# Kernel tuning notes

Hardware: AMD Instinct MI355X
Metric: run time of the kernel (lower is better)

## Reference

```python
import jax, jax.numpy as jnp
import numpy as np

S, N, IN_F, OUT_F = 8, 2048, 256, 64
SLOPE = 0.1
NEG_INF = -9e15


def leaky_relu(x, slope=SLOPE):
    return jnp.where(x >= 0, x, slope * x)


def setup_inputs() -> dict:
    key = jax.random.key(0)
    k1, k2, k3, k4, k5, k6 = jax.random.split(key, 6)
    inDoc = jax.random.normal(k1, (S, N, IN_F), dtype=jnp.float32)
    adj = jax.random.randint(k2, (S, N, N, 1), 0, 2, dtype=jnp.int32)
    # Linear(inFeat, outFeat): weight [outFeat, inFeat], bias [outFeat]
    W_w = jax.random.normal(k3, (OUT_F, IN_F), dtype=jnp.float32) / np.sqrt(IN_F)
    W_b = jax.random.normal(k4, (OUT_F,), dtype=jnp.float32) * 0.01
    # Linear(2*outFeat, 1): weight [1, 2*outFeat], bias [1]
    a_w = jax.random.normal(k5, (1, 2 * OUT_F), dtype=jnp.float32) / np.sqrt(2 * OUT_F)
    a_b = jax.random.normal(k6, (1,), dtype=jnp.float32) * 0.01
    return {"inDoc": inDoc, "adj": adj, "W_w": W_w, "W_b": W_b, "a_w": a_w, "a_b": a_b}


def reference(inDoc, adj, W_w, W_b, a_w, a_b):
    # h: [S, N, F]
    h = jnp.einsum('snd,fd->snf', inDoc, W_w) + W_b
    F_ = h.shape[-1]
    # aParams(concat(h_i, h_j)) == h_i @ a1 + h_j @ a2 + b  (exact same affine map)
    a1 = a_w[0, :F_]
    a2 = a_w[0, F_:]
    score_i = jnp.einsum('snf,f->sn', h, a1)  # [S, N]
    score_j = jnp.einsum('snf,f->sn', h, a2)  # [S, N]
    att = score_i[:, :, None] + score_j[:, None, :] + a_b[0]  # [S, N, N]
    att = leaky_relu(att)
    m = adj[..., 0]  # [S, N, N]
    att = jnp.where((m == 0) | (m == -1), jnp.float32(NEG_INF), att)
    att = jax.nn.softmax(att, axis=2)  # normalize over neighbors j
    h_out = leaky_relu(jnp.einsum('sij,sjf->sif', att, h))
    return (h_out, att)
```

## Files before the change

kernel.cpp:

```cpp
#include <hip/hip_runtime.h>

#define SLOPE 0.1f
#define NEG_INF_F (-9000000000000000.0f)

typedef int            iv4    __attribute__((ext_vector_type(4)));
typedef float          fv4    __attribute__((ext_vector_type(4)));
typedef unsigned short u16;
typedef u16            u16v4  __attribute__((ext_vector_type(4)));
typedef __bf16         bf16x8 __attribute__((ext_vector_type(8)));

static __device__ __forceinline__ u16 f2bf(float x) {
    union { float f; unsigned u; } v; v.f = x;
    unsigned r = v.u + 0x7fffu + ((v.u >> 16) & 1u);
    return (u16)(r >> 16);
}

static __device__ __forceinline__ void lds_barrier() {
    asm volatile("s_waitcnt lgkmcnt(0)" ::: "memory");
    __builtin_amdgcn_s_barrier();
}


__global__ void k_wt(const float* __restrict__ W, float* __restrict__ wT) {
    int idx = blockIdx.x * 256 + threadIdx.x;
    int k = idx >> 6, f = idx & 63;
    wT[idx] = W[f * 256 + k];
}

__global__ __launch_bounds__(256) void k_h(
    const float* __restrict__ inDoc, const float* __restrict__ wT,
    const float* __restrict__ Wb, const float* __restrict__ aw,
    u16* __restrict__ hT, float* __restrict__ si, float* __restrict__ sj)
{
    __shared__ float wTl[32 * 64];
    __shared__ float inl[32][36];
    const int t  = threadIdx.x;
    const int R0 = blockIdx.x * 32;
    const int fq = t & 15, rq = t >> 4;
    const int f0 = fq << 2;

    float acc[2][4];
#pragma unroll
    for (int r = 0; r < 2; ++r)
#pragma unroll
        for (int c = 0; c < 4; ++c) acc[r][c] = 0.f;

    for (int kc = 0; kc < 8; ++kc) {
        __syncthreads();
        {
            const float4* src = (const float4*)(wT + kc * 2048);
            float4 a = src[t * 2], b = src[t * 2 + 1];
            ((float4*)wTl)[t * 2]     = a;
            ((float4*)wTl)[t * 2 + 1] = b;
        }
        {
            int r = t >> 3, q = t & 7;
            const float* src = inDoc + (size_t)(R0 + r) * 256 + kc * 32 + q * 4;
            *(float4*)&inl[r][q * 4] = *(const float4*)src;
        }
        __syncthreads();
#pragma unroll
        for (int k4 = 0; k4 < 8; ++k4) {
            const int k0 = k4 << 2;
            float w[4][4];
#pragma unroll
            for (int j = 0; j < 4; ++j) {
                float4 wv = *(const float4*)&wTl[(k0 + j) * 64 + f0];
                w[j][0] = wv.x; w[j][1] = wv.y; w[j][2] = wv.z; w[j][3] = wv.w;
            }
#pragma unroll
            for (int r = 0; r < 2; ++r) {
                float4 av = *(const float4*)&inl[rq * 2 + r][k0];
                float a[4] = {av.x, av.y, av.z, av.w};
#pragma unroll
                for (int j = 0; j < 4; ++j)
#pragma unroll
                    for (int c = 0; c < 4; ++c)
                        acc[r][c] = fmaf(a[j], w[j][c], acc[r][c]);
            }
        }
    }

    float bw[4], a1[4], a2[4];
#pragma unroll
    for (int c = 0; c < 4; ++c) {
        bw[c] = Wb[f0 + c];
        a1[c] = aw[f0 + c];
        a2[c] = aw[64 + f0 + c];
    }
    float sip[2], sjp[2];
#pragma unroll
    for (int r = 0; r < 2; ++r) {
#pragma unroll
        for (int c = 0; c < 4; ++c) acc[r][c] += bw[c];
        float x = 0.f, y = 0.f;
#pragma unroll
        for (int c = 0; c < 4; ++c) {
            x = fmaf(acc[r][c], a1[c], x);
            y = fmaf(acc[r][c], a2[c], y);
        }
        sip[r] = x; sjp[r] = y;
    }
#pragma unroll
    for (int m = 1; m <= 8; m <<= 1) {
#pragma unroll
        for (int r = 0; r < 2; ++r) {
            sip[r] += __shfl_xor(sip[r], m, 64);
            sjp[r] += __shfl_xor(sjp[r], m, 64);
        }
    }
    const int rowbase = R0 + rq * 2;
    const int sR = rowbase >> 11;
    const int il = rowbase & 2047;
    u16* hTp = hT + (size_t)sR * 131072;
#pragma unroll
    for (int r = 0; r < 2; ++r)
#pragma unroll
        for (int c = 0; c < 4; ++c)
            hTp[(size_t)(f0 + c) * 2048 + il + r] = f2bf(acc[r][c]);
    if (fq == 0) {
#pragma unroll
        for (int r = 0; r < 2; ++r) {
            si[rowbase + r] = sip[r];
            sj[rowbase + r] = sjp[r];
        }
    }
}

__global__ __launch_bounds__(512, 2) void k_att(
    const int* __restrict__ adj, const u16* __restrict__ hT,
    const float* __restrict__ si, const float* __restrict__ sj,
    const float* __restrict__ ab_p,
    float* __restrict__ out_h, float* __restrict__ out_att)
{
    __shared__ __align__(16) u16 pB[16 * 2048];
    __shared__ __align__(16) float red[4][64][4];
    const int t    = threadIdx.x;
    const int lane = t & 63, wv = t >> 6;
    const int i0   = blockIdx.x * 16;
    const int s    = i0 >> 11;
    const float ab = ab_p[0];
    const float* sjb = sj + (size_t)s * 2048;

    fv4 sv[8];
#pragma unroll
    for (int c = 0; c < 8; ++c)
        sv[c] = *(const fv4*)(sjb + c * 256 + lane * 4);

    const int r0  = wv * 2,      r1  = r0 + 1;
    const int fr0 = i0 + r0,     fr1 = i0 + r1;
    const float si0 = si[fr0] + ab;
    const float si1 = si[fr1] + ab;
    const int* a0 = adj + (size_t)fr0 * 2048;
    const int* a1 = adj + (size_t)fr1 * 2048;

    iv4 m0[8], m1[8];
#pragma unroll
    for (int c = 0; c < 8; ++c)
        m0[c] = __builtin_nontemporal_load((const iv4*)(a0 + c * 256 + lane * 4));
#pragma unroll
    for (int c = 0; c < 8; ++c)
        m1[c] = __builtin_nontemporal_load((const iv4*)(a1 + c * 256 + lane * 4));

#pragma unroll
    for (int rr = 0; rr < 2; ++rr) {
        const int r  = rr ? r1 : r0;
        const int fr = rr ? fr1 : fr0;
        const float sival = rr ? si1 : si0;
        iv4* mm = rr ? m1 : m0;
        float v[32];
#pragma unroll
        for (int c = 0; c < 8; ++c) {
            iv4 m = mm[c];
            float x;
            x = sival + sv[c].x; x = fmaxf(x, SLOPE * x);
            v[c*4+0] = (m.x == 0 || m.x == -1) ? NEG_INF_F : x;
            x = sival + sv[c].y; x = fmaxf(x, SLOPE * x);
            v[c*4+1] = (m.y == 0 || m.y == -1) ? NEG_INF_F : x;
            x = sival + sv[c].z; x = fmaxf(x, SLOPE * x);
            v[c*4+2] = (m.z == 0 || m.z == -1) ? NEG_INF_F : x;
            x = sival + sv[c].w; x = fmaxf(x, SLOPE * x);
            v[c*4+3] = (m.w == 0 || m.w == -1) ? NEG_INF_F : x;
        }
        float mx = v[0];
#pragma unroll
        for (int q = 1; q < 32; ++q) mx = fmaxf(mx, v[q]);
#pragma unroll
        for (int m2 = 1; m2 < 64; m2 <<= 1) mx = fmaxf(mx, __shfl_xor(mx, m2, 64));
        float sum = 0.f;
#pragma unroll
        for (int q = 0; q < 32; ++q) { v[q] = __expf(v[q] - mx); sum += v[q]; }
#pragma unroll
        for (int m2 = 1; m2 < 64; m2 <<= 1) sum += __shfl_xor(sum, m2, 64);
        const float inv = 1.0f / sum;

        float* attrow = out_att + (size_t)fr * 2048;
        const unsigned swz = (unsigned)(r & 7) << 4;
#pragma unroll
        for (int c = 0; c < 8; ++c) {
            const int j = c * 256 + lane * 4;
            fv4 pv;
            pv.x = v[c*4+0] * inv; pv.y = v[c*4+1] * inv;
            pv.z = v[c*4+2] * inv; pv.w = v[c*4+3] * inv;
            *(fv4*)(attrow + j) = pv;
            u16v4 pk;
            pk.x = f2bf(pv.x); pk.y = f2bf(pv.y);
            pk.z = f2bf(pv.z); pk.w = f2bf(pv.w);
            unsigned byte = ((unsigned)(r * 4096 + j * 2)) ^ swz;
            *(u16v4*)((char*)pB + byte) = pk;
        }
    }
    lds_barrier();

    const int fq    = wv & 3;
    const int kh    = wv >> 2;
    const int m16   = lane & 15;
    const int klane = lane >> 4;
    const unsigned sw = (unsigned)(lane & 7) << 4;
    const __bf16* hTs = (const __bf16*)hT + (size_t)s * 131072
                      + (size_t)(fq * 16 + m16) * 2048 + kh * 1024 + klane * 8;
    const unsigned bbase = (unsigned)(m16 * 4096 + kh * 2048 + klane * 16);
    fv4 acc = {0.f, 0.f, 0.f, 0.f};
#pragma unroll 4
    for (int k0 = 0; k0 < 1024; k0 += 32) {
        bf16x8 a = *(const bf16x8*)(hTs + k0);
        unsigned byte = (bbase + (unsigned)(k0 * 2)) ^ sw;
        bf16x8 b = *(const bf16x8*)((const char*)pB + byte);
        acc = __builtin_amdgcn_mfma_f32_16x16x32_bf16(a, b, acc, 0, 0, 0);
    }
    if (kh == 1)
        *(fv4*)&red[fq][lane][0] = acc;
    lds_barrier();
    if (kh == 0) {
        fv4 p2 = *(const fv4*)&red[fq][lane][0];
        acc += p2;
        const int orow = i0 + m16;
        float* op = out_h + (size_t)orow * 64 + fq * 16 + klane * 4;
        fv4 o;
        o.x = fmaxf(acc.x, SLOPE * acc.x);
        o.y = fmaxf(acc.y, SLOPE * acc.y);
        o.z = fmaxf(acc.z, SLOPE * acc.z);
        o.w = fmaxf(acc.w, SLOPE * acc.w);
        *(fv4*)op = o;
    }
}

extern "C" void kernel_launch(void* const* d_in, const int* in_sizes, int n_in,
                              void* d_out, int out_size, void* d_ws, size_t ws_size,
                              hipStream_t stream) {
    const float* inDoc = (const float*)d_in[0];
    const int*   adj   = (const int*)d_in[1];
    const float* W_w   = (const float*)d_in[2];
    const float* W_b   = (const float*)d_in[3];
    const float* a_w   = (const float*)d_in[4];
    const float* a_b   = (const float*)d_in[5];

    float* out     = (float*)d_out;
    float* out_h   = out;
    float* out_att = out + (size_t)16384 * 64;

    float* ws = (float*)d_ws;
    float* wT = ws;
    u16*   hT = (u16*)(ws + 16384);
    float* si = (float*)(hT + (size_t)8 * 64 * 2048);
    float* sj = si + 16384;

    k_wt <<<64,   256, 0, stream>>>(W_w, wT);
    k_h  <<<512,  256, 0, stream>>>(inDoc, wT, W_b, a_w, hT, si, sj);
    k_att<<<1024, 512, 0, stream>>>(adj, hT, si, sj, a_b, out_h, out_att);
}
```

Baseline: 91.08 us.

## Process two row tiles per block and prefetch next tile's adjacency

Each attention block now handles 32 rows as two 16-row tiles, with half as many blocks launched. While the first tile's softmax, stores and MFMA run, the adjacency rows for the second tile are loaded into registers, so their latency can overlap with compute. The cost is higher register pressure (prefetched masks plus two score arrays) under a 128-VGPR bound, which could cause spills. There is also less block-level parallelism to hide latency across the device.

```diff
diff --git a/kernel.cpp b/kernel.cpp
--- a/kernel.cpp
+++ b/kernel.cpp
@@ -137,8 +137,8 @@
     __shared__ __align__(16) float red[4][64][4];
     const int t    = threadIdx.x;
     const int lane = t & 63, wv = t >> 6;
-    const int i0   = blockIdx.x * 16;
-    const int s    = i0 >> 11;
+    const int base = blockIdx.x * 32;
+    const int s    = base >> 11;
     const float ab = ab_p[0];
     const float* sjb = sj + (size_t)s * 2048;
 
@@ -146,71 +146,6 @@
 #pragma unroll
     for (int c = 0; c < 8; ++c)
         sv[c] = *(const fv4*)(sjb + c * 256 + lane * 4);
-
-    const int r0  = wv * 2,      r1  = r0 + 1;
-    const int fr0 = i0 + r0,     fr1 = i0 + r1;
-    const float si0 = si[fr0] + ab;
-    const float si1 = si[fr1] + ab;
-    const int* a0 = adj + (size_t)fr0 * 2048;
-    const int* a1 = adj + (size_t)fr1 * 2048;
-
-    iv4 m0[8], m1[8];
-#pragma unroll
-    for (int c = 0; c < 8; ++c)
-        m0[c] = __builtin_nontemporal_load((const iv4*)(a0 + c * 256 + lane * 4));
-#pragma unroll
-    for (int c = 0; c < 8; ++c)
-        m1[c] = __builtin_nontemporal_load((const iv4*)(a1 + c * 256 + lane * 4));
-
-#pragma unroll
-    for (int rr = 0; rr < 2; ++rr) {
-        const int r  = rr ? r1 : r0;
-        const int fr = rr ? fr1 : fr0;
-        const float sival = rr ? si1 : si0;
-        iv4* mm = rr ? m1 : m0;
-        float v[32];
-#pragma unroll
-        for (int c = 0; c < 8; ++c) {
-            iv4 m = mm[c];
-            float x;
-            x = sival + sv[c].x; x = fmaxf(x, SLOPE * x);
-            v[c*4+0] = (m.x == 0 || m.x == -1) ? NEG_INF_F : x;
-            x = sival + sv[c].y; x = fmaxf(x, SLOPE * x);
-            v[c*4+1] = (m.y == 0 || m.y == -1) ? NEG_INF_F : x;
-            x = sival + sv[c].z; x = fmaxf(x, SLOPE * x);
-            v[c*4+2] = (m.z == 0 || m.z == -1) ? NEG_INF_F : x;
-            x = sival + sv[c].w; x = fmaxf(x, SLOPE * x);
-            v[c*4+3] = (m.w == 0 || m.w == -1) ? NEG_INF_F : x;
-        }
-        float mx = v[0];
-#pragma unroll
-        for (int q = 1; q < 32; ++q) mx = fmaxf(mx, v[q]);
-#pragma unroll
-        for (int m2 = 1; m2 < 64; m2 <<= 1) mx = fmaxf(mx, __shfl_xor(mx, m2, 64));
-        float sum = 0.f;
-#pragma unroll
-        for (int q = 0; q < 32; ++q) { v[q] = __expf(v[q] - mx); sum += v[q]; }
-#pragma unroll
-        for (int m2 = 1; m2 < 64; m2 <<= 1) sum += __shfl_xor(sum, m2, 64);
-        const float inv = 1.0f / sum;
-
-        float* attrow = out_att + (size_t)fr * 2048;
-        const unsigned swz = (unsigned)(r & 7) << 4;
-#pragma unroll
-        for (int c = 0; c < 8; ++c) {
-            const int j = c * 256 + lane * 4;
-            fv4 pv;
-            pv.x = v[c*4+0] * inv; pv.y = v[c*4+1] * inv;
-            pv.z = v[c*4+2] * inv; pv.w = v[c*4+3] * inv;
-            *(fv4*)(attrow + j) = pv;
-            u16v4 pk;
-            pk.x = f2bf(pv.x); pk.y = f2bf(pv.y);
-            pk.z = f2bf(pv.z); pk.w = f2bf(pv.w);
-            unsigned byte = ((unsigned)(r * 4096 + j * 2)) ^ swz;
-            *(u16v4*)((char*)pB + byte) = pk;
-        }
-    }
-    lds_barrier();
 
     const int fq    = wv & 3;
     const int kh    = wv >> 2;
@@ -220,28 +155,125 @@
     const __bf16* hTs = (const __bf16*)hT + (size_t)s * 131072
                       + (size_t)(fq * 16 + m16) * 2048 + kh * 1024 + klane * 8;
     const unsigned bbase = (unsigned)(m16 * 4096 + kh * 2048 + klane * 16);
-    fv4 acc = {0.f, 0.f, 0.f, 0.f};
+
+    iv4 mc[16];
+    {
+        const int fr0 = base + wv * 2, fr1 = fr0 + 1;
+        const int* a0 = adj + (size_t)fr0 * 2048;
+        const int* a1 = adj + (size_t)fr1 * 2048;
+#pragma unroll
+        for (int c = 0; c < 8; ++c)
+            mc[c]     = __builtin_nontemporal_load((const iv4*)(a0 + c * 256 + lane * 4));
+#pragma unroll
+        for (int c = 0; c < 8; ++c)
+            mc[8 + c] = __builtin_nontemporal_load((const iv4*)(a1 + c * 256 + lane * 4));
+    }
+
+#pragma unroll 2
+    for (int tile = 0; tile < 2; ++tile) {
+        const int ti0 = base + tile * 16;
+        const int r0  = wv * 2, r1 = r0 + 1;
+        const float si0 = si[ti0 + r0] + ab;
+        const float si1 = si[ti0 + r1] + ab;
+
+        float v0[32], v1[32];
+#pragma unroll
+        for (int c = 0; c < 8; ++c) {
+            iv4 m = mc[c];
+            float x;
+            x = si0 + sv[c].x; x = fmaxf(x, SLOPE * x);
+            v0[c*4+0] = (m.x == 0 || m.x == -1) ? NEG_INF_F : x;
+            x = si0 + sv[c].y; x = fmaxf(x, SLOPE * x);
+            v0[c*4+1] = (m.y == 0 || m.y == -1) ? NEG_INF_F : x;
+            x = si0 + sv[c].z; x = fmaxf(x, SLOPE * x);
+            v0[c*4+2] = (m.z == 0 || m.z == -1) ? NEG_INF_F : x;
+            x = si0 + sv[c].w; x = fmaxf(x, SLOPE * x);
+            v0[c*4+3] = (m.w == 0 || m.w == -1) ? NEG_INF_F : x;
+        }
+#pragma unroll
+        for (int c = 0; c < 8; ++c) {
+            iv4 m = mc[8 + c];
+            float x;
+            x = si1 + sv[c].x; x = fmaxf(x, SLOPE * x);
+            v1[c*4+0] = (m.x == 0 || m.x == -1) ? NEG_INF_F : x;
+            x = si1 + sv[c].y; x = fmaxf(x, SLOPE * x);
+            v1[c*4+1] = (m.y == 0 || m.y == -1) ? NEG_INF_F : x;
+            x = si1 + sv[c].z; x = fmaxf(x, SLOPE * x);
+            v1[c*4+2] = (m.z == 0 || m.z == -1) ? NEG_INF_F : x;
+            x = si1 + sv[c].w; x = fmaxf(x, SLOPE * x);
+            v1[c*4+3] = (m.w == 0 || m.w == -1) ? NEG_INF_F : x;
+        }
+
+        if (tile == 0) {
+            const int fr0n = base + 16 + wv * 2, fr1n = fr0n + 1;
+            const int* a0 = adj + (size_t)fr0n * 2048;
+            const int* a1 = adj + (size_t)fr1n * 2048;
+#pragma unroll
+            for (int c = 0; c < 8; ++c)
+                mc[c]     = __builtin_nontemporal_load((const iv4*)(a0 + c * 256 + lane * 4));
+#pragma unroll
+            for (int c = 0; c < 8; ++c)
+                mc[8 + c] = __builtin_nontemporal_load((const iv4*)(a1 + c * 256 + lane * 4));
+        }
+
+#pragma unroll
+        for (int rr = 0; rr < 2; ++rr) {
+            float* v = rr ? v1 : v0;
+            const int r  = rr ? r1 : r0;
+            const int fr = ti0 + r;
+            float mx = v[0];
+#pragma unroll
+            for (int q = 1; q < 32; ++q) mx = fmaxf(mx, v[q]);
+#pragma unroll
+            for (int m2 = 1; m2 < 64; m2 <<= 1) mx = fmaxf(mx, __shfl_xor(mx, m2, 64));
+            float sum = 0.f;
+#pragma unroll
+            for (int q = 0; q < 32; ++q) { v[q] = __expf(v[q] - mx); sum += v[q]; }
+#pragma unroll
+            for (int m2 = 1; m2 < 64; m2 <<= 1) sum += __shfl_xor(sum, m2, 64);
+            const float inv = 1.0f / sum;
+
+            float* attrow = out_att + (size_t)fr * 2048;
+            const unsigned swz = (unsigned)(r & 7) << 4;
+#pragma unroll
+            for (int c = 0; c < 8; ++c) {
+                const int j = c * 256 + lane * 4;
+                fv4 pv;
+                pv.x = v[c*4+0] * inv; pv.y = v[c*4+1] * inv;
+                pv.z = v[c*4+2] * inv; pv.w = v[c*4+3] * inv;
+                *(fv4*)(attrow + j) = pv;
+                u16v4 pk;
+                pk.x = f2bf(pv.x); pk.y = f2bf(pv.y);
+                pk.z = f2bf(pv.z); pk.w = f2bf(pv.w);
+                unsigned byte = ((unsigned)(r * 4096 + j * 2)) ^ swz;
+                *(u16v4*)((char*)pB + byte) = pk;
+            }
+        }
+        lds_barrier();
+
+        fv4 acc = {0.f, 0.f, 0.f, 0.f};
 #pragma unroll 4
-    for (int k0 = 0; k0 < 1024; k0 += 32) {
-        bf16x8 a = *(const bf16x8*)(hTs + k0);
-        unsigned byte = (bbase + (unsigned)(k0 * 2)) ^ sw;
-        bf16x8 b = *(const bf16x8*)((const char*)pB + byte);
-        acc = __builtin_amdgcn_mfma_f32_16x16x32_bf16(a, b, acc, 0, 0, 0);
-    }
-    if (kh == 1)
-        *(fv4*)&red[fq][lane][0] = acc;
-    lds_barrier();
-    if (kh == 0) {
-        fv4 p2 = *(const fv4*)&red[fq][lane][0];
-        acc += p2;
-        const int orow = i0 + m16;
-        float* op = out_h + (size_t)orow * 64 + fq * 16 + klane * 4;
-        fv4 o;
-        o.x = fmaxf(acc.x, SLOPE * acc.x);
-        o.y = fmaxf(acc.y, SLOPE * acc.y);
-        o.z = fmaxf(acc.z, SLOPE * acc.z);
-        o.w = fmaxf(acc.w, SLOPE * acc.w);
-        *(fv4*)op = o;
+        for (int k0 = 0; k0 < 1024; k0 += 32) {
+            bf16x8 a = *(const bf16x8*)(hTs + k0);
+            unsigned byte = (bbase + (unsigned)(k0 * 2)) ^ sw;
+            bf16x8 b = *(const bf16x8*)((const char*)pB + byte);
+            acc = __builtin_amdgcn_mfma_f32_16x16x32_bf16(a, b, acc, 0, 0, 0);
+        }
+        if (kh == 1)
+            *(fv4*)&red[fq][lane][0] = acc;
+        lds_barrier();
+        if (kh == 0) {
+            fv4 p2 = *(const fv4*)&red[fq][lane][0];
+            acc += p2;
+            const int orow = ti0 + m16;
+            float* op = out_h + (size_t)orow * 64 + fq * 16 + klane * 4;
+            fv4 o;
+            o.x = fmaxf(acc.x, SLOPE * acc.x);
+            o.y = fmaxf(acc.y, SLOPE * acc.y);
+            o.z = fmaxf(acc.z, SLOPE * acc.z);
+            o.w = fmaxf(acc.w, SLOPE * acc.w);
+            *(fv4*)op = o;
+        }
     }
 }
 
@@ -265,7 +297,7 @@
     float* si = (float*)(hT + (size_t)8 * 64 * 2048);
     float* sj = si + 16384;
 
-    k_wt <<<64,   256, 0, stream>>>(W_w, wT);
-    k_h  <<<512,  256, 0, stream>>>(inDoc, wT, W_b, a_w, hT, si, sj);
-    k_att<<<1024, 512, 0, stream>>>(adj, hT, si, sj, a_b, out_h, out_att);
-}
+    k_wt <<<64,  256, 0, stream>>>(W_w, wT);
+    k_h  <<<512, 256, 0, stream>>>(inDoc, wT, W_b, a_w, hT, si, sj);
+    k_att<<<512, 512, 0, stream>>>(adj, hT, si, sj, a_b, out_h, out_att);
+}
```

Measured after the change: 96.67 us. 6.1% more time.

## Stage adjacency rows into LDS via direct global-to-LDS loads, reuse buffer for probabilities

Applied to the files above, without the earlier changes.

Adjacency rows are now loaded with global_load_lds straight into a 128KB LDS buffer instead of into registers. After the mask is read, the same per-row buffer is reused in place to hold the bf16 softmax probabilities for the MFMA stage. The attention output store is made nontemporal. The larger LDS footprint forces occupancy down to one block per CU, trading latency hiding for lower register pressure and an asynchronous load path.

```diff
diff --git a/kernel.cpp b/kernel.cpp
--- a/kernel.cpp
+++ b/kernel.cpp
@@ -18,6 +18,12 @@
 static __device__ __forceinline__ void lds_barrier() {
     asm volatile("s_waitcnt lgkmcnt(0)" ::: "memory");
     __builtin_amdgcn_s_barrier();
+}
+
+typedef __attribute__((address_space(1))) const void gv1;
+typedef __attribute__((address_space(3))) void lv3;
+static __device__ __forceinline__ void gload_lds16(const void* g, void* l) {
+    __builtin_amdgcn_global_load_lds((gv1*)g, (lv3*)l, 16, 0, 0);
 }
 
 
@@ -127,13 +133,13 @@
     }
 }
 
-__global__ __launch_bounds__(512, 2) void k_att(
+__global__ __launch_bounds__(512, 1) void k_att(
     const int* __restrict__ adj, const u16* __restrict__ hT,
     const float* __restrict__ si, const float* __restrict__ sj,
     const float* __restrict__ ab_p,
     float* __restrict__ out_h, float* __restrict__ out_att)
 {
-    __shared__ __align__(16) u16 pB[16 * 2048];
+    __shared__ __align__(16) int   adjL[16 * 2048];
     __shared__ __align__(16) float red[4][64][4];
     const int t    = threadIdx.x;
     const int lane = t & 63, wv = t >> 6;
@@ -147,31 +153,35 @@
     for (int c = 0; c < 8; ++c)
         sv[c] = *(const fv4*)(sjb + c * 256 + lane * 4);
 
-    const int r0  = wv * 2,      r1  = r0 + 1;
-    const int fr0 = i0 + r0,     fr1 = i0 + r1;
+    const int r0  = wv * 2, r1 = r0 + 1;
+    const int fr0 = i0 + r0, fr1 = i0 + r1;
     const float si0 = si[fr0] + ab;
     const float si1 = si[fr1] + ab;
-    const int* a0 = adj + (size_t)fr0 * 2048;
-    const int* a1 = adj + (size_t)fr1 * 2048;
-
-    iv4 m0[8], m1[8];
-#pragma unroll
-    for (int c = 0; c < 8; ++c)
-        m0[c] = __builtin_nontemporal_load((const iv4*)(a0 + c * 256 + lane * 4));
-#pragma unroll
-    for (int c = 0; c < 8; ++c)
-        m1[c] = __builtin_nontemporal_load((const iv4*)(a1 + c * 256 + lane * 4));
+
+    {
+        const int* a0 = adj + (size_t)fr0 * 2048;
+        const int* a1 = adj + (size_t)fr1 * 2048;
+        int* L0 = &adjL[r0 * 2048];
+        int* L1 = &adjL[r1 * 2048];
+#pragma unroll
+        for (int c = 0; c < 8; ++c)
+            gload_lds16(a0 + c * 256 + lane * 4, L0 + c * 256);
+#pragma unroll
+        for (int c = 0; c < 8; ++c)
+            gload_lds16(a1 + c * 256 + lane * 4, L1 + c * 256);
+    }
 
 #pragma unroll
     for (int rr = 0; rr < 2; ++rr) {
+        asm volatile("s_waitcnt vmcnt(8)" ::: "memory");
         const int r  = rr ? r1 : r0;
         const int fr = rr ? fr1 : fr0;
         const float sival = rr ? si1 : si0;
-        iv4* mm = rr ? m1 : m0;
+        const int* Lrow = &adjL[r * 2048];
         float v[32];
 #pragma unroll
         for (int c = 0; c < 8; ++c) {
-            iv4 m = mm[c];
+            iv4 m = *(const iv4*)(Lrow + c * 256 + lane * 4);
             float x;
             x = sival + sv[c].x; x = fmaxf(x, SLOPE * x);
             v[c*4+0] = (m.x == 0 || m.x == -1) ? NEG_INF_F : x;
@@ -195,6 +205,7 @@
         const float inv = 1.0f / sum;
 
         float* attrow = out_att + (size_t)fr * 2048;
+        u16* prow = (u16*)&adjL[r * 2048];
         const unsigned swz = (unsigned)(r & 7) << 4;
 #pragma unroll
         for (int c = 0; c < 8; ++c) {
@@ -202,12 +213,12 @@
             fv4 pv;
             pv.x = v[c*4+0] * inv; pv.y = v[c*4+1] * inv;
             pv.z = v[c*4+2] * inv; pv.w = v[c*4+3] * inv;
-            *(fv4*)(attrow + j) = pv;
+            __builtin_nontemporal_store(pv, (fv4*)(attrow + j));
             u16v4 pk;
             pk.x = f2bf(pv.x); pk.y = f2bf(pv.y);
             pk.z = f2bf(pv.z); pk.w = f2bf(pv.w);
-            unsigned byte = ((unsigned)(r * 4096 + j * 2)) ^ swz;
-            *(u16v4*)((char*)pB + byte) = pk;
+            unsigned byte = ((unsigned)(j * 2)) ^ swz;
+            *(u16v4*)((char*)prow + byte) = pk;
         }
     }
     lds_barrier();
@@ -216,16 +227,18 @@
     const int kh    = wv >> 2;
     const int m16   = lane & 15;
     const int klane = lane >> 4;
-    const unsigned sw = (unsigned)(lane & 7) << 4;
+    const unsigned sw = (unsigned)(m16 & 7) << 4;
     const __bf16* hTs = (const __bf16*)hT + (size_t)s * 131072
                       + (size_t)(fq * 16 + m16) * 2048 + kh * 1024 + klane * 8;
-    const unsigned bbase = (unsigned)(m16 * 4096 + kh * 2048 + klane * 16);
+    const char* pBc = (const char*)adjL;
+    const unsigned bbase = (unsigned)(m16 * 8192) ;
+    const unsigned koff0 = (unsigned)(kh * 2048 + klane * 16);
     fv4 acc = {0.f, 0.f, 0.f, 0.f};
 #pragma unroll 4
     for (int k0 = 0; k0 < 1024; k0 += 32) {
         bf16x8 a = *(const bf16x8*)(hTs + k0);
-        unsigned byte = (bbase + (unsigned)(k0 * 2)) ^ sw;
-        bf16x8 b = *(const bf16x8*)((const char*)pB + byte);
+        unsigned byte = bbase + ((koff0 + (unsigned)(k0 * 2)) ^ sw);
+        bf16x8 b = *(const bf16x8*)(pBc + byte);
         acc = __builtin_amdgcn_mfma_f32_16x16x32_bf16(a, b, acc, 0, 0, 0);
     }
     if (kh == 1)
```

After: 93.02 us. +2.1%, slower.
